# Optimization experiments

Hardware: AMD Instinct MI355X
Metric: run time of the kernel (lower is better)

The kernel has to match this reference:

```python
import jax, jax.numpy as jnp
import numpy as np

B, N, MAX_T, NUM_CLASSES = 128, 1024, 64, 80
PRED_DIM = 5 + NUM_CLASSES  # 85; cls logits are pred[:, 6:] per the source (79 classes)


def setup_inputs() -> dict:
    key = jax.random.key(0)
    k1, k2, k3 = jax.random.split(key, 3)
    preds = jax.random.normal(k1, (B, N, PRED_DIM), dtype=jnp.float32)
    # well-formed boxes: two random corners per target, sorted so x1<=x2, y1<=y2
    corners = jax.random.uniform(k2, (B, MAX_T, 2, 2), dtype=jnp.float32)
    lo = jnp.min(corners, axis=2)
    hi = jnp.max(corners, axis=2)
    # class id in [-1, 78]; -1 marks an invalid (padded) target
    cls_id = jax.random.randint(k3, (B, MAX_T), -1, NUM_CLASSES - 1).astype(jnp.float32)
    targets = jnp.concatenate([lo, hi, cls_id[..., None]], axis=-1)  # (B, MAX_T, 5)
    return {"preds": preds, "targets": targets}


def _pairwise_iou(pb, tb):
    # pb: (N,4), tb: (M,4) -> (N,M)
    x1 = jnp.maximum(pb[:, None, 0], tb[None, :, 0])
    y1 = jnp.maximum(pb[:, None, 1], tb[None, :, 1])
    x2 = jnp.minimum(pb[:, None, 2], tb[None, :, 2])
    y2 = jnp.minimum(pb[:, None, 3], tb[None, :, 3])
    inter = jnp.clip(x2 - x1, 0.0) * jnp.clip(y2 - y1, 0.0)
    a1 = (pb[:, 2] - pb[:, 0]) * (pb[:, 3] - pb[:, 1])
    a2 = (tb[:, 2] - tb[:, 0]) * (tb[:, 3] - tb[:, 1])
    union = a1[:, None] + a2[None, :] - inter
    return inter / (union + 1e-6)


def _loss_one(pred, tgt):
    n = pred.shape[0]
    valid = tgt[:, 4] >= 0.0                      # (M,)
    kv = valid.sum()
    ious = _pairwise_iou(pred[:, :4], tgt[:, :4])  # (N,M)
    ious = jnp.where(valid[None, :], ious, -1.0)   # invalid targets never match
    best_ious = ious.max(axis=1)                   # (N,)
    best_idx = ious.argmax(axis=1)                 # (N,)
    matched_raw = best_ious > 0.5
    matched = jnp.where(matched_raw.any(), matched_raw, best_ious == best_ious.max())
    m = matched.astype(pred.dtype)
    u = 1.0 - m
    mcnt = m.sum()
    ucnt = u.sum()

    mt = tgt[best_idx]                             # (N,5) matched targets
    # SmoothL1 (beta=1), masked mean over matched rows x 4 coords
    d = pred[:, :4] - mt[:, :4]
    ad = jnp.abs(d)
    sl1 = jnp.where(ad < 1.0, 0.5 * d * d, ad - 0.5)
    bbox_loss = (sl1 * m[:, None]).sum() / jnp.maximum(mcnt * 4.0, 1.0)

    # cross entropy over pred[:, 6:] (faithful to source slicing)
    logits = pred[:, 6:]
    labels = jnp.clip(mt[:, 4].astype(jnp.int32), 0, logits.shape[1] - 1)
    ce = jax.nn.logsumexp(logits, axis=-1) - jnp.take_along_axis(logits, labels[:, None], axis=1)[:, 0]
    cls_loss = (ce * m).sum() / jnp.maximum(mcnt, 1.0)

    conf_logit = pred[:, 4]
    conf_m = (jax.nn.softplus(-conf_logit) * m).sum() / jnp.maximum(mcnt, 1.0)  # BCE vs 1
    conf_u = (jax.nn.softplus(conf_logit) * u).sum() / jnp.maximum(ucnt, 1.0)   # BCE vs 0
    conf_loss = jnp.where(ucnt > 0, (conf_m + conf_u) * 0.5, conf_m)

    loss_valid = bbox_loss + cls_loss + conf_loss
    loss_novalid = jax.nn.softplus(conf_logit).mean()  # BCE vs all-zero targets
    return jnp.where(kv > 0, loss_valid, loss_novalid)


def reference(preds, targets):
    per_sample = jax.vmap(_loss_one)(preds, targets)  # (B,)
    return per_sample.sum() / preds.shape[0]
```

## Files before the change

### kernel.cpp

```cpp
#include <hip/hip_runtime.h>
#include <math.h>

#define NPRED 1024
#define NT 64
#define PD 85
#define NLOGIT 79
#define QBLK 8
#define RPB 128
#define THREADS 256

__device__ __forceinline__ float softplusf(float x) {
    return fmaxf(x, 0.0f) + log1pf(expf(-fabsf(x)));
}


__global__ __launch_bounds__(THREADS)
void k1_match(const float* __restrict__ preds,
              const float* __restrict__ targets,
              float* __restrict__ part, int nblk)
{
    const int bx   = blockIdx.x;
    const int b    = bx >> 3;
    const int q    = bx & 7;
    const int tid  = threadIdx.x;
    const int row  = tid >> 1;
    const int half = tid & 1;
    const int r    = q * RPB + row;

    __shared__ float  tgs[NT * 5];
    __shared__ float4 tb[NT];
    __shared__ float  tcl[NT];
    __shared__ unsigned long long vmask_s;
    __shared__ float  red[4][11];
    __shared__ float  redm[4];
    __shared__ float  bmax_s;

    const float* pp = preds + ((size_t)b * NPRED + r) * PD;
    const float px1 = pp[0], py1 = pp[1], px2 = pp[2], py2 = pp[3], conf = pp[4];

    if (tid < (NT * 5 / 4))
        ((float4*)tgs)[tid] = ((const float4*)(targets + (size_t)b * NT * 5))[tid];
    __syncthreads();
    if (tid < NT) {
        float a = tgs[tid*5], c = tgs[tid*5+1], d = tgs[tid*5+2], e = tgs[tid*5+3], f = tgs[tid*5+4];
        tb[tid]  = make_float4(a, c, d, e);
        tcl[tid] = f;
        unsigned long long bl = __ballot(f >= 0.0f);
        if (tid == 0) vmask_s = bl;
    }
    __syncthreads();

    const unsigned long long vmask = vmask_s;

    const float parea = (px2 - px1) * (py2 - py1);
    const int t0 = half * 32;
    float best = -INFINITY;
    int   bidx = t0;
    #pragma unroll 8
    for (int i = 0; i < 32; ++i) {
        const int t = t0 + i;
        const float4 tt = tb[t];
        float w = fminf(px2, tt.z) - fmaxf(px1, tt.x); w = fmaxf(w, 0.0f);
        float h = fminf(py2, tt.w) - fmaxf(py1, tt.y); h = fmaxf(h, 0.0f);
        float inter = w * h;
        float ta    = (tt.z - tt.x) * (tt.w - tt.y);
        float uni   = parea + ta - inter;
        float iou   = ((vmask >> t) & 1ULL) ? inter / (uni + 1e-6f) : -1.0f;
        if (iou > best) { best = iou; bidx = t; }
    }

    const float obest = __shfl_xor(best, 1);
    const int   obidx = __shfl_xor(bidx, 1);
    const float bA = half ? obest : best;
    const int   iA = half ? obidx : bidx;
    const float bB = half ? best  : obest;
    const int   iB = half ? bidx  : obidx;
    const float fbest = (bA >= bB) ? bA : bB;
    const int   fidx  = (bA >= bB) ? iA : iB;

    {
        float v = fbest;
        #pragma unroll
        for (int o = 32; o > 0; o >>= 1) v = fmaxf(v, __shfl_down(v, o));
        if ((tid & 63) == 0) redm[tid >> 6] = v;
        __syncthreads();
        if (tid == 0) bmax_s = fmaxf(fmaxf(redm[0], redm[1]), fmaxf(redm[2], redm[3]));
        __syncthreads();
    }
    const float bmax = bmax_s;
    const bool cA = (fbest > 0.5f);
    const bool cB = (fbest == bmax);

    const float sp = softplusf(conf);
    float vals[11];
    #pragma unroll
    for (int j = 0; j < 11; ++j) vals[j] = 0.0f;
    if (half == 0) vals[0] = sp;

    if (cA || cB) {
        const float* lg = pp + 6;
        const int base = half * 40;
        const int len  = half ? 39 : 40;
        float m = -INFINITY, s = 0.0f;
        #pragma unroll 8
        for (int i = 0; i < len; ++i) {
            float v  = lg[base + i];
            float nm = fmaxf(m, v);
            s = s * expf(m - nm) + expf(v - nm);
            m = nm;
        }
        const float om = __shfl_xor(m, 1);
        const float os = __shfl_xor(s, 1);
        const float nm = fmaxf(m, om);
        const float st = s * expf(m - nm) + os * expf(om - nm);
        const float lse = nm + logf(st);

        if (half == 0) {
            const float4 mt = tb[fidx];
            float dd[4] = { px1 - mt.x, py1 - mt.y, px2 - mt.z, py2 - mt.w };
            float bb = 0.0f;
            #pragma unroll
            for (int i = 0; i < 4; ++i) {
                float ad = fabsf(dd[i]);
                bb += (ad < 1.0f) ? 0.5f * dd[i] * dd[i] : ad - 0.5f;
            }
            int label = (int)tcl[fidx];
            label = label < 0 ? 0 : (label > NLOGIT - 1 ? NLOGIT - 1 : label);
            const float cev = lse - lg[label];
            const float sfm = softplusf(-conf);

            if (cA) { vals[1] += 1.0f; vals[2] += bb; vals[3] += cev; vals[4] += sfm; vals[5] += sp; }
            if (cB) { vals[6] += 1.0f; vals[7] += bb; vals[8] += cev; vals[9] += sfm; vals[10] += sp; }
        }
    }

    #pragma unroll
    for (int j = 0; j < 11; ++j) {
        float v = vals[j];
        #pragma unroll
        for (int o = 32; o > 0; o >>= 1) v += __shfl_down(v, o);
        if ((tid & 63) == 0) red[tid >> 6][j] = v;
    }
    __syncthreads();
    if (tid < 11)  part[(size_t)tid * nblk + bx] = red[0][tid] + red[1][tid] + red[2][tid] + red[3][tid];
    if (tid == 11) part[(size_t)11  * nblk + bx] = bmax;
    if (tid == 12) part[(size_t)12  * nblk + bx] = (float)__popcll(vmask);
}

__global__ __launch_bounds__(1024)
void k2_final(const float* __restrict__ part, float* __restrict__ out,
              int nb, int nblk)
{
    const int t = threadIdx.x;
    const int s = t >> 3, k = t & 7;
    const int bx = s * 8 + k;

    __shared__ float ps[128];
    __shared__ float r2[2];

    float v[13];
    #pragma unroll
    for (int j = 0; j < 13; ++j) v[j] = part[(size_t)j * nblk + bx];

    float gmax = v[11];
    #pragma unroll
    for (int o = 1; o < 8; o <<= 1) gmax = fmaxf(gmax, __shfl_xor(gmax, o));
    const float mB = (v[11] == gmax) ? 1.0f : 0.0f;
    #pragma unroll
    for (int j = 6; j <= 10; ++j) v[j] *= mB;
    #pragma unroll
    for (int j = 0; j < 11; ++j) {
        #pragma unroll
        for (int o = 1; o < 8; o <<= 1) v[j] += __shfl_xor(v[j], o);
    }

    if (k == 0 && s < nb) {
        const float sp_total = v[0];
        const bool  anym = (v[1] > 0.0f);
        const float mcnt = anym ? v[1] : v[6];
        const float bboxs= anym ? v[2] : v[7];
        const float ces  = anym ? v[3] : v[8];
        const float sfms = anym ? v[4] : v[9];
        const float spms = anym ? v[5] : v[10];
        const float ucnt = (float)NPRED - mcnt;
        const float sfus = sp_total - spms;
        const float bbox_loss = bboxs / fmaxf(mcnt * 4.0f, 1.0f);
        const float cls_loss  = ces   / fmaxf(mcnt, 1.0f);
        const float conf_m    = sfms  / fmaxf(mcnt, 1.0f);
        const float conf_u    = sfus  / fmaxf(ucnt, 1.0f);
        const float conf_loss = (ucnt > 0.0f) ? (conf_m + conf_u) * 0.5f : conf_m;
        const float loss_valid   = bbox_loss + cls_loss + conf_loss;
        const float loss_novalid = sp_total / (float)NPRED;
        const int   kv = (int)v[12];
        ps[s] = (kv > 0) ? loss_valid : loss_novalid;
    }
    __syncthreads();

    if (t < 128) {
        float x = (t < nb) ? ps[t] : 0.0f;
        #pragma unroll
        for (int o = 32; o > 0; o >>= 1) x += __shfl_down(x, o);
        if ((t & 63) == 0) r2[t >> 6] = x;
    }
    __syncthreads();
    if (t == 0) out[0] = (r2[0] + r2[1]) / (float)nb;
}

extern "C" void kernel_launch(void* const* d_in, const int* in_sizes, int n_in,
                              void* d_out, int out_size, void* d_ws, size_t ws_size,
                              hipStream_t stream) {
    const float* preds   = (const float*)d_in[0];
    const float* targets = (const float*)d_in[1];
    float* out  = (float*)d_out;
    float* part = (float*)d_ws;

    const int nb   = in_sizes[0] / (NPRED * PD);
    const int nblk = nb * QBLK;

    hipLaunchKernelGGL(k1_match, dim3(nblk), dim3(THREADS), 0, stream,
                       preds, targets, part, nblk);
    hipLaunchKernelGGL(k2_final, dim3(1), dim3(1024), 0, stream,
                       part, out, nb, nblk);
}
```

Measured before the change: 31.48 us.

## Stage each block's prediction slab into LDS via direct global-to-LDS loads

The block's contiguous 128x85 float slab of predictions is now copied into shared memory with coalesced 16-byte global_load_lds instructions, and later reads take the box, conf and logits from LDS. Before, each thread issued scattered strided global loads per row. This replaces uncoalesced global reads with coalesced bulk transfers, but it adds about 43 KB of LDS per block, which lowers occupancy, and the whole slab is loaded even when few rows are matched. It also relies on the __syncthreads after the target load to cover completion of the async LDS loads.

```diff
diff --git a/kernel.cpp b/kernel.cpp
--- a/kernel.cpp
+++ b/kernel.cpp
@@ -8,9 +8,19 @@
 #define QBLK 8
 #define RPB 128
 #define THREADS 256
+#define SLAB_DW (RPB * PD)
+#define SLAB_F4 (SLAB_DW / 4)
+#define FULL_IT 10
+#define TAIL_BASE (SLAB_F4 - THREADS)
 
 __device__ __forceinline__ float softplusf(float x) {
     return fmaxf(x, 0.0f) + log1pf(expf(-fabsf(x)));
+}
+
+__device__ __forceinline__ void load_lds16(const float4* g, float4* l) {
+    __builtin_amdgcn_global_load_lds((const __attribute__((address_space(1))) void*)g,
+                                     (__attribute__((address_space(3))) void*)l,
+                                     16, 0, 0);
 }
 
 
@@ -25,8 +35,9 @@
     const int tid  = threadIdx.x;
     const int row  = tid >> 1;
     const int half = tid & 1;
-    const int r    = q * RPB + row;
-
+    const int wbase = tid & 192;
+
+    __shared__ float  slab[SLAB_DW];
     __shared__ float  tgs[NT * 5];
     __shared__ float4 tb[NT];
     __shared__ float  tcl[NT];
@@ -35,12 +46,19 @@
     __shared__ float  redm[4];
     __shared__ float  bmax_s;
 
-    const float* pp = preds + ((size_t)b * NPRED + r) * PD;
-    const float px1 = pp[0], py1 = pp[1], px2 = pp[2], py2 = pp[3], conf = pp[4];
-
-    if (tid < (NT * 5 / 4))
-        ((float4*)tgs)[tid] = ((const float4*)(targets + (size_t)b * NT * 5))[tid];
-    __syncthreads();
+    const float4* g4 = (const float4*)(preds + ((size_t)b * NPRED + (size_t)q * RPB) * PD);
+    float4* s4 = (float4*)slab;
+    #pragma unroll
+    for (int i = 0; i < FULL_IT; ++i) {
+        load_lds16(g4 + i * THREADS + tid, s4 + i * THREADS + wbase);
+    }
+    load_lds16(g4 + TAIL_BASE + tid, s4 + TAIL_BASE + wbase);
+
+    float4 tg4;
+    if (tid < (NT * 5 / 4)) tg4 = ((const float4*)(targets + (size_t)b * NT * 5))[tid];
+    if (tid < (NT * 5 / 4)) ((float4*)tgs)[tid] = tg4;
+    __syncthreads();
+
     if (tid < NT) {
         float a = tgs[tid*5], c = tgs[tid*5+1], d = tgs[tid*5+2], e = tgs[tid*5+3], f = tgs[tid*5+4];
         tb[tid]  = make_float4(a, c, d, e);
@@ -51,6 +69,9 @@
     __syncthreads();
 
     const unsigned long long vmask = vmask_s;
+    const float px1 = slab[row*PD+0], py1 = slab[row*PD+1];
+    const float px2 = slab[row*PD+2], py2 = slab[row*PD+3];
+    const float conf = slab[row*PD+4];
 
     const float parea = (px2 - px1) * (py2 - py1);
     const int t0 = half * 32;
@@ -98,7 +119,7 @@
     if (half == 0) vals[0] = sp;
 
     if (cA || cB) {
-        const float* lg = pp + 6;
+        const float* lg = &slab[row * PD + 6];
         const int base = half * 40;
         const int len  = half ? 39 : 40;
         float m = -INFINITY, s = 0.0f;
```

Result: slower. 37.30 us (+18.5%).
